# Performance work log

Measured on AMD Instinct MI355X. Metric: run time of the kernel, lower is better.

Reference implementation:

```python
import jax, jax.numpy as jnp
import numpy as np

NUM_HEADS = 8
BN_EPS = 1e-5


def setup_inputs() -> dict:
    key = jax.random.key(0)
    ks = jax.random.split(key, 8)
    B, Ct, Cs, H, W, E = 8, 256, 128, 32, 32, 256
    s = 0.05  # small init scale to keep softmax logits reasonable
    return {
        "tgt": jax.random.normal(ks[0], (B, Ct, H, W), jnp.float32),
        "src": jax.random.normal(ks[1], (B, Cs, H, W), jnp.float32),
        "kv_w": jax.random.normal(ks[2], (E, Cs), jnp.float32) * s,
        "in_proj_w": jax.random.normal(ks[3], (3 * E, E), jnp.float32) * s,
        "in_proj_b": jnp.zeros((3 * E,), jnp.float32),
        "out_proj_w": jax.random.normal(ks[4], (E, E), jnp.float32) * s,
        "out_proj_b": jnp.zeros((E,), jnp.float32),
        "fuse_w": jax.random.normal(ks[5], (Ct, E), jnp.float32) * s,
        "bn_gamma": jnp.ones((Ct,), jnp.float32),
        "bn_beta": jnp.zeros((Ct,), jnp.float32),
        "bn_mean": jnp.zeros((Ct,), jnp.float32),
        "bn_var": jnp.ones((Ct,), jnp.float32),
    }


def reference(tgt, src, kv_w, in_proj_w, in_proj_b, out_proj_w, out_proj_b,
              fuse_w, bn_gamma, bn_beta, bn_mean, bn_var):
    B, Ct, H, W = tgt.shape
    E = kv_w.shape[0]
    nH = NUM_HEADS
    hd = E // nH

    # q_proj is Identity (C_tgt == embed_dim); flatten spatial to tokens [B, Q, E]
    q_seq = tgt.reshape(B, Ct, H * W).transpose(0, 2, 1)
    # kv_proj: 1x1 conv == channel matmul; then flatten to [B, K, E]
    kv_map = jnp.einsum('bchw,ec->behw', src, kv_w)
    k_seq = kv_map.reshape(B, E, H * W).transpose(0, 2, 1)

    # nn.MultiheadAttention: packed in-projection
    Wq, Wk, Wv = in_proj_w[:E], in_proj_w[E:2 * E], in_proj_w[2 * E:]
    bq, bk, bv = in_proj_b[:E], in_proj_b[E:2 * E], in_proj_b[2 * E:]
    qp = (q_seq @ Wq.T + bq).reshape(B, -1, nH, hd).transpose(0, 2, 1, 3)  # [B,h,Q,d]
    kp = (k_seq @ Wk.T + bk).reshape(B, -1, nH, hd).transpose(0, 2, 1, 3)  # [B,h,K,d]
    vp = (k_seq @ Wv.T + bv).reshape(B, -1, nH, hd).transpose(0, 2, 1, 3)  # [B,h,K,d]

    scores = jnp.einsum('bhqd,bhkd->bhqk', qp, kp) / jnp.sqrt(jnp.float32(hd))
    attn = jax.nn.softmax(scores, axis=-1)  # [B,h,Q,K] (non-flash explicit path)

    ctx = jnp.einsum('bhqk,bhkd->bhqd', attn, vp)
    ctx = ctx.transpose(0, 2, 1, 3).reshape(B, -1, E)  # [B,Q,E]
    out_seq = ctx @ out_proj_w.T + out_proj_b

    # cached spatial key-attention map: mean over heads and queries -> [B,1,Hk,Wk]
    attn_map = attn.mean(axis=(1, 2)).reshape(B, 1, H, W)

    # back to map, fuse: 1x1 conv -> BN(eval) -> SiLU, then residual add
    out_map = out_seq.transpose(0, 2, 1).reshape(B, E, H, W)
    fused = jnp.einsum('behw,ce->bchw', out_map, fuse_w)
    inv = bn_gamma / jnp.sqrt(bn_var + BN_EPS)
    bn = (fused - bn_mean[None, :, None, None]) * inv[None, :, None, None] \
         + bn_beta[None, :, None, None]
    y = tgt + bn * jax.nn.sigmoid(bn)  # SiLU
    return y, attn_map
```

## Files before the change

kernel.cpp:

```cpp
#include <hip/hip_runtime.h>
#include <hip/hip_bf16.h>

typedef unsigned short u16;
typedef __attribute__((ext_vector_type(8))) short short8;
typedef __attribute__((ext_vector_type(4))) float f32x4;
typedef __attribute__((ext_vector_type(4))) unsigned short u16x4;

static __device__ __forceinline__ u16 f2bf(float x) {
  __hip_bfloat16 b = __float2bfloat16(x);
  return *reinterpret_cast<u16*>(&b);
}

#define QSCALE 0.17677669529663687f

__global__ __launch_bounds__(256) void prep_kernel(
    const float* __restrict__ in_proj_w, const float* __restrict__ in_proj_b,
    const float* __restrict__ kv_w, const float* __restrict__ fuse_w,
    const float* __restrict__ out_proj_w, const float* __restrict__ out_proj_b,
    const float* __restrict__ gamma, const float* __restrict__ beta,
    const float* __restrict__ mean, const float* __restrict__ var,
    u16* __restrict__ WqB, u16* __restrict__ WkvB, u16* __restrict__ M2B,
    float* __restrict__ qbias, float2* __restrict__ bnpk) {
  int idx = blockIdx.x * 256 + threadIdx.x;
  if (idx < 65536) {
    WqB[idx] = f2bf(in_proj_w[idx] * QSCALE);
  } else if (idx < 131072) {
    int i = idx - 65536;
    int m = i >> 7, c = i & 127;
    const float* wrow = in_proj_w + (size_t)(256 + m) * 256;
    float s = 0.f;
    for (int e2 = 0; e2 < 256; ++e2) s += wrow[e2] * kv_w[e2 * 128 + c];
    WkvB[i] = f2bf(s);
  } else if (idx < 196608) {
    int i = idx - 131072;
    int c = i >> 8, e2 = i & 255;
    float s = 0.f;
    for (int e = 0; e < 256; ++e)
      s += fuse_w[c * 256 + e] * out_proj_w[e * 256 + e2];
    M2B[i] = f2bf(s);
  } else if (idx < 196864) {
    int c = idx - 196608;
    float fbv = 0.f;
    for (int e = 0; e < 256; ++e) fbv += fuse_w[c * 256 + e] * out_proj_b[e];
    float inv = gamma[c] * rsqrtf(var[c] + 1e-5f);
    bnpk[c] = make_float2(inv, (fbv - mean[c]) * inv + beta[c]);
    qbias[c] = in_proj_b[c] * QSCALE;
  }
}

__global__ __launch_bounds__(256, 3) void qkv_gemm(
    const float* __restrict__ tgt, const float* __restrict__ src,
    const u16* __restrict__ WqB, const u16* __restrict__ WkvB,
    const float* __restrict__ qbias, const float* __restrict__ bkv,
    u16* __restrict__ QB, u16* __restrict__ KB, u16* __restrict__ VB) {
  __shared__ __align__(16) u16 Wl[64 * 40];
  __shared__ __align__(16) u16 Xl[128 * 40];
  int b = blockIdx.z, by = blockIdx.y, n0 = blockIdx.x * 128;
  bool isQ = by < 4;
  int m0 = isQ ? by * 64 : (by - 4) * 64;
  int Kd = isQ ? 256 : 128;
  const u16* Wp = isQ ? WqB : WkvB;
  const float* Xp = isQ ? tgt + (size_t)b * 256 * 1024
                        : src + (size_t)b * 128 * 1024;
  int t = threadIdx.x, wave = t >> 6, lane = t & 63;
  int lq = lane & 15, quad = lane >> 4;
  f32x4 acc[4][2];
#pragma unroll
  for (int mt = 0; mt < 4; ++mt)
#pragma unroll
    for (int nt = 0; nt < 2; ++nt) acc[mt][nt] = (f32x4){0.f, 0.f, 0.f, 0.f};

  for (int k0 = 0; k0 < Kd; k0 += 32) {
    __syncthreads();
    {
      int row = t >> 2, seg = t & 3;
      *(short8*)&Wl[row * 40 + seg * 8] =
          *(const short8*)&Wp[(size_t)(m0 + row) * Kd + k0 + seg * 8];
    }
    for (int i = t; i < 4096; i += 256) {
      int k = i >> 7, n = i & 127;
      Xl[n * 40 + k] = f2bf(Xp[(size_t)(k0 + k) * 1024 + n0 + n]);
    }
    __syncthreads();
    short8 af[4], bf[2];
#pragma unroll
    for (int mt = 0; mt < 4; ++mt)
      af[mt] = *(const short8*)&Wl[(mt * 16 + lq) * 40 + quad * 8];
#pragma unroll
    for (int nt = 0; nt < 2; ++nt)
      bf[nt] = *(const short8*)&Xl[(wave * 32 + nt * 16 + lq) * 40 + quad * 8];
#pragma unroll
    for (int mt = 0; mt < 4; ++mt)
#pragma unroll
      for (int nt = 0; nt < 2; ++nt)
        acc[mt][nt] = __builtin_amdgcn_mfma_f32_16x16x32_bf16(af[mt], bf[nt],
                                                              acc[mt][nt], 0, 0, 0);
  }
  if (isQ) {
#pragma unroll
    for (int mt = 0; mt < 4; ++mt) {
      int e = m0 + mt * 16 + quad * 4;
      f32x4 bi = *(const f32x4*)&qbias[e];
#pragma unroll
      for (int nt = 0; nt < 2; ++nt) {
        int n = n0 + wave * 32 + nt * 16 + lq;
        u16x4 pk;
#pragma unroll
        for (int r = 0; r < 4; ++r) pk[r] = f2bf(acc[mt][nt][r] + bi[r]);
        *(u16x4*)&QB[((size_t)b * 1024 + n) * 256 + e] = pk;
      }
    }
  } else {
#pragma unroll
    for (int mt = 0; mt < 4; ++mt) {
      int m = m0 + mt * 16 + quad * 4;
      f32x4 bi = *(const f32x4*)&bkv[m];
#pragma unroll
      for (int nt = 0; nt < 2; ++nt) {
        int n = n0 + wave * 32 + nt * 16 + lq;
        if (m < 256) {
          int hh = m >> 5, d = m & 31;
          u16x4 pk;
#pragma unroll
          for (int r = 0; r < 4; ++r) pk[r] = f2bf(acc[mt][nt][r] + bi[r]);
          *(u16x4*)&KB[((size_t)(b * 8 + hh) * 1024 + n) * 32 + d] = pk;
        } else {
          int e = m - 256;
#pragma unroll
          for (int r = 0; r < 4; ++r)
            VB[((size_t)b * 256 + e + r) * 1024 + n] = f2bf(acc[mt][nt][r] + bi[r]);
        }
      }
    }
  }
}

__global__ __launch_bounds__(256, 4) void attn_mfma(
    const u16* __restrict__ QB, const u16* __restrict__ KB,
    const u16* __restrict__ VB, u16* __restrict__ ctxB,
    float* __restrict__ attn_out) {
  __shared__ __align__(16) u16 Klds[128 * 40];
  __shared__ __align__(16) u16 Vlds[32 * 136];
  __shared__ __align__(16) u16 Plds[4][32 * 40];
  __shared__ float colsum[1024];

  int b = blockIdx.z, h = blockIdx.y, q0 = blockIdx.x * 128;
  int t = threadIdx.x, wave = t >> 6, lane = t & 63;
  int lq = lane & 15, quad = lane >> 4;

  const u16* Qb = QB + (size_t)b * 1024 * 256 + h * 32;
  const u16* Kb = KB + (size_t)(b * 8 + h) * 1024 * 32;
  const u16* Vb = VB + (size_t)(b * 256 + h * 32) * 1024;

  short8 qf[2];
#pragma unroll
  for (int mt = 0; mt < 2; ++mt)
    qf[mt] = *(const short8*)(Qb + (size_t)(q0 + wave * 32 + mt * 16 + lq) * 256 + quad * 8);

  for (int i = t; i < 1024; i += 256) colsum[i] = 0.f;

  float lsum[2][4];
  f32x4 O[2][2];
#pragma unroll
  for (int mt = 0; mt < 2; ++mt) {
#pragma unroll
    for (int r = 0; r < 4; ++r) lsum[mt][r] = 0.f;
#pragma unroll
    for (int nt = 0; nt < 2; ++nt) O[mt][nt] = (f32x4){0.f, 0.f, 0.f, 0.f};
  }
  const f32x4 zf = (f32x4){0.f, 0.f, 0.f, 0.f};
  u16* Pw = &Plds[wave][0];

  for (int c0 = 0; c0 < 1024; c0 += 128) {
    __syncthreads();
    for (int i = t; i < 512; i += 256)
      *(short8*)&Klds[(i >> 2) * 40 + (i & 3) * 8] =
          *(const short8*)(Kb + (size_t)c0 * 32 + i * 8);
    for (int i = t; i < 512; i += 256) {
      int d = i >> 4, part = i & 15;
      *(short8*)&Vlds[d * 136 + part * 8] =
          *(const short8*)(Vb + (size_t)d * 1024 + c0 + part * 8);
    }
    __syncthreads();
#pragma unroll
    for (int pair = 0; pair < 4; ++pair) {
#pragma unroll
      for (int ntp = 0; ntp < 2; ++ntp) {
        int nt = pair * 2 + ntp;
        short8 kf = *(const short8*)&Klds[(nt * 16 + lq) * 40 + quad * 8];
#pragma unroll
        for (int mt = 0; mt < 2; ++mt) {
          f32x4 s = __builtin_amdgcn_mfma_f32_16x16x32_bf16(qf[mt], kf, zf, 0, 0, 0);
#pragma unroll
          for (int r = 0; r < 4; ++r) {
            float e = __expf(s[r]);
            lsum[mt][r] += e;
            Pw[(mt * 16 + quad * 4 + r) * 40 + ntp * 16 + lq] = f2bf(e);
          }
        }
      }
      short8 pf[2], vf[2];
#pragma unroll
      for (int mt = 0; mt < 2; ++mt)
        pf[mt] = *(const short8*)&Pw[(mt * 16 + lq) * 40 + quad * 8];
#pragma unroll
      for (int nt = 0; nt < 2; ++nt)
        vf[nt] = *(const short8*)&Vlds[(nt * 16 + lq) * 136 + pair * 32 + quad * 8];
#pragma unroll
      for (int mt = 0; mt < 2; ++mt)
#pragma unroll
        for (int nt = 0; nt < 2; ++nt)
          O[mt][nt] = __builtin_amdgcn_mfma_f32_16x16x32_bf16(pf[mt], vf[nt],
                                                              O[mt][nt], 0, 0, 0);
    }
  }

  float linv[2][4];
#pragma unroll
  for (int mt = 0; mt < 2; ++mt)
#pragma unroll
    for (int r = 0; r < 4; ++r) {
      float v = lsum[mt][r];
      v += __shfl_xor(v, 1);
      v += __shfl_xor(v, 2);
      v += __shfl_xor(v, 4);
      v += __shfl_xor(v, 8);
      linv[mt][r] = 1.f / v;
    }

#pragma unroll
  for (int mt = 0; mt < 2; ++mt)
#pragma unroll
    for (int nt = 0; nt < 2; ++nt)
#pragma unroll
      for (int r = 0; r < 4; ++r) {
        int q = q0 + wave * 32 + mt * 16 + quad * 4 + r;
        ctxB[((size_t)b * 1024 + q) * 256 + h * 32 + nt * 16 + lq] =
            f2bf(O[mt][nt][r] * linv[mt][r]);
      }

  for (int c0 = 0; c0 < 1024; c0 += 128) {
    __syncthreads();
    for (int i = t; i < 512; i += 256)
      *(short8*)&Klds[(i >> 2) * 40 + (i & 3) * 8] =
          *(const short8*)(Kb + (size_t)c0 * 32 + i * 8);
    __syncthreads();
#pragma unroll
    for (int nt = 0; nt < 8; ++nt) {
      short8 kf = *(const short8*)&Klds[(nt * 16 + lq) * 40 + quad * 8];
      float cs = 0.f;
#pragma unroll
      for (int mt = 0; mt < 2; ++mt) {
        f32x4 s = __builtin_amdgcn_mfma_f32_16x16x32_bf16(qf[mt], kf, zf, 0, 0, 0);
#pragma unroll
        for (int r = 0; r < 4; ++r) cs += __expf(s[r]) * linv[mt][r];
      }
      cs += __shfl_xor(cs, 16);
      cs += __shfl_xor(cs, 32);
      if (quad == 0) atomicAdd(&colsum[c0 + nt * 16 + lq], cs);
    }
  }
  __syncthreads();
  for (int i = t; i < 1024; i += 256)
    atomicAdd(&attn_out[b * 1024 + i], colsum[i] * (1.f / 8192.f));
}

__global__ __launch_bounds__(256, 3) void fused_out(
    const u16* __restrict__ M2B, const u16* __restrict__ ctxB,
    const float* __restrict__ tgt, const float2* __restrict__ bnpk,
    float* __restrict__ y) {
  __shared__ __align__(16) u16 Al[64 * 40];
  __shared__ __align__(16) u16 Bl[128 * 40];
  int b = blockIdx.z, c0 = blockIdx.y * 64, s0 = blockIdx.x * 128;
  int t = threadIdx.x, wave = t >> 6, lane = t & 63;
  int lq = lane & 15, quad = lane >> 4;
  f32x4 acc[4][2];
#pragma unroll
  for (int mt = 0; mt < 4; ++mt)
#pragma unroll
    for (int nt = 0; nt < 2; ++nt) acc[mt][nt] = (f32x4){0.f, 0.f, 0.f, 0.f};

  for (int k0 = 0; k0 < 256; k0 += 32) {
    __syncthreads();
    {
      int row = t >> 2, seg = t & 3;
      *(short8*)&Al[row * 40 + seg * 8] =
          *(const short8*)&M2B[(size_t)(c0 + row) * 256 + k0 + seg * 8];
    }
    for (int i = t; i < 512; i += 256) {
      int row = i >> 2, seg = i & 3;
      *(short8*)&Bl[row * 40 + seg * 8] =
          *(const short8*)&ctxB[((size_t)b * 1024 + s0 + row) * 256 + k0 + seg * 8];
    }
    __syncthreads();
    short8 af[4], bf[2];
#pragma unroll
    for (int mt = 0; mt < 4; ++mt)
      af[mt] = *(const short8*)&Al[(mt * 16 + lq) * 40 + quad * 8];
#pragma unroll
    for (int nt = 0; nt < 2; ++nt)
      bf[nt] = *(const short8*)&Bl[(wave * 32 + nt * 16 + lq) * 40 + quad * 8];
#pragma unroll
    for (int mt = 0; mt < 4; ++mt)
#pragma unroll
      for (int nt = 0; nt < 2; ++nt)
        acc[mt][nt] = __builtin_amdgcn_mfma_f32_16x16x32_bf16(af[mt], bf[nt],
                                                              acc[mt][nt], 0, 0, 0);
  }
#pragma unroll
  for (int mt = 0; mt < 4; ++mt) {
#pragma unroll
    for (int r = 0; r < 4; ++r) {
      int c = c0 + mt * 16 + quad * 4 + r;
      float2 p = bnpk[c];
#pragma unroll
      for (int nt = 0; nt < 2; ++nt) {
        int s = s0 + wave * 32 + nt * 16 + lq;
        float bn = acc[mt][nt][r] * p.x + p.y;
        float sig = 1.f / (1.f + __expf(-bn));
        size_t idx = ((size_t)b * 256 + c) * 1024 + s;
        y[idx] = tgt[idx] + bn * sig;
      }
    }
  }
}

extern "C" void kernel_launch(void* const* d_in, const int* in_sizes, int n_in,
                              void* d_out, int out_size, void* d_ws, size_t ws_size,
                              hipStream_t stream) {
  const float* tgt = (const float*)d_in[0];
  const float* src = (const float*)d_in[1];
  const float* kv_w = (const float*)d_in[2];
  const float* in_proj_w = (const float*)d_in[3];
  const float* in_proj_b = (const float*)d_in[4];
  const float* out_proj_w = (const float*)d_in[5];
  const float* out_proj_b = (const float*)d_in[6];
  const float* fuse_w = (const float*)d_in[7];
  const float* bn_gamma = (const float*)d_in[8];
  const float* bn_beta = (const float*)d_in[9];
  const float* bn_mean = (const float*)d_in[10];
  const float* bn_var = (const float*)d_in[11];

  char* W = (char*)d_ws;
  u16* WqB = (u16*)W;
  u16* WkvB = (u16*)(W + 131072);
  u16* M2B = (u16*)(W + 262144);
  float* qbias = (float*)(W + 393216);
  float2* bnpk = (float2*)(W + 394240);
  u16* QB = (u16*)(W + 397312);
  u16* KB = QB + 2097152;
  u16* VB = KB + 2097152;
  u16* ctxB = VB + 2097152;

  float* y = (float*)d_out;
  float* attn_out = y + 2097152;

  hipMemsetAsync(attn_out, 0, 8192 * sizeof(float), stream);
  prep_kernel<<<769, 256, 0, stream>>>(in_proj_w, in_proj_b, kv_w, fuse_w,
                                       out_proj_w, out_proj_b, bn_gamma, bn_beta,
                                       bn_mean, bn_var, WqB, WkvB, M2B, qbias, bnpk);
  qkv_gemm<<<dim3(8, 12, 8), 256, 0, stream>>>(tgt, src, WqB, WkvB, qbias,
                                               in_proj_b + 256, QB, KB, VB);
  attn_mfma<<<dim3(8, 8, 8), 256, 0, stream>>>(QB, KB, VB, ctxB, attn_out);
  fused_out<<<dim3(8, 4, 8), 256, 0, stream>>>(M2B, ctxB, tgt, bnpk, y);
}
```

Measured before the change: 176.9 us.

## Rewrite attention as register-resident S^T MFMA loop without LDS staging

The attention kernel now computes transposed score tiles (K as the A operand, Q as B), so the exp'd probabilities land in registers already laid out as the B operand of the PV MFMA. That removes the LDS round trip for P and the LDS staging of K and V, which now load straight from global memory. The log2(e) factor is folded into the Q scale so exp2f can replace __expf, and bf16 packing truncates with a byte-permute instead of rounding. Each block now covers 64 queries (16 per wave) over twice as many blocks, trading lower register pressure and no barriers in the main loop for repeated global K/V reads and slightly less accurate bf16 P values.

```diff
diff --git a/kernel.cpp b/kernel.cpp
--- a/kernel.cpp
+++ b/kernel.cpp
@@ -2,16 +2,24 @@
 #include <hip/hip_bf16.h>
 
 typedef unsigned short u16;
+typedef unsigned int u32;
 typedef __attribute__((ext_vector_type(8))) short short8;
 typedef __attribute__((ext_vector_type(4))) float f32x4;
 typedef __attribute__((ext_vector_type(4))) unsigned short u16x4;
+typedef __attribute__((ext_vector_type(4))) int i32x4;
 
 static __device__ __forceinline__ u16 f2bf(float x) {
   __hip_bfloat16 b = __float2bfloat16(x);
   return *reinterpret_cast<u16*>(&b);
 }
-
-#define QSCALE 0.17677669529663687f
+static __device__ __forceinline__ u32 fbits(float x) {
+  union { float f; u32 u; } v; v.f = x; return v.u;
+}
+static __device__ __forceinline__ u32 pk_trunc(float lo, float hi) {
+  return __builtin_amdgcn_perm(fbits(hi), fbits(lo), 0x07060302u);
+}
+
+#define QSCALE2 (0.17677669529663687f * 1.4426950408889634f)
 
 __global__ __launch_bounds__(256) void prep_kernel(
     const float* __restrict__ in_proj_w, const float* __restrict__ in_proj_b,
@@ -23,7 +31,7 @@
     float* __restrict__ qbias, float2* __restrict__ bnpk) {
   int idx = blockIdx.x * 256 + threadIdx.x;
   if (idx < 65536) {
-    WqB[idx] = f2bf(in_proj_w[idx] * QSCALE);
+    WqB[idx] = f2bf(in_proj_w[idx] * QSCALE2);
   } else if (idx < 131072) {
     int i = idx - 65536;
     int m = i >> 7, c = i & 127;
@@ -44,7 +52,7 @@
     for (int e = 0; e < 256; ++e) fbv += fuse_w[c * 256 + e] * out_proj_b[e];
     float inv = gamma[c] * rsqrtf(var[c] + 1e-5f);
     bnpk[c] = make_float2(inv, (fbv - mean[c]) * inv + beta[c]);
-    qbias[c] = in_proj_b[c] * QSCALE;
+    qbias[c] = in_proj_b[c] * QSCALE2;
   }
 }
 
@@ -135,16 +143,12 @@
   }
 }
 
-__global__ __launch_bounds__(256, 4) void attn_mfma(
+__global__ __launch_bounds__(256) void attn_st(
     const u16* __restrict__ QB, const u16* __restrict__ KB,
     const u16* __restrict__ VB, u16* __restrict__ ctxB,
     float* __restrict__ attn_out) {
-  __shared__ __align__(16) u16 Klds[128 * 40];
-  __shared__ __align__(16) u16 Vlds[32 * 136];
-  __shared__ __align__(16) u16 Plds[4][32 * 40];
   __shared__ float colsum[1024];
-
-  int b = blockIdx.z, h = blockIdx.y, q0 = blockIdx.x * 128;
+  int b = blockIdx.z, h = blockIdx.y, q0 = blockIdx.x * 64;
   int t = threadIdx.x, wave = t >> 6, lane = t & 63;
   int lq = lane & 15, quad = lane >> 4;
 
@@ -152,113 +156,77 @@
   const u16* Kb = KB + (size_t)(b * 8 + h) * 1024 * 32;
   const u16* Vb = VB + (size_t)(b * 256 + h * 32) * 1024;
 
-  short8 qf[2];
-#pragma unroll
-  for (int mt = 0; mt < 2; ++mt)
-    qf[mt] = *(const short8*)(Qb + (size_t)(q0 + wave * 32 + mt * 16 + lq) * 256 + quad * 8);
-
   for (int i = t; i < 1024; i += 256) colsum[i] = 0.f;
 
-  float lsum[2][4];
-  f32x4 O[2][2];
-#pragma unroll
-  for (int mt = 0; mt < 2; ++mt) {
-#pragma unroll
-    for (int r = 0; r < 4; ++r) lsum[mt][r] = 0.f;
-#pragma unroll
-    for (int nt = 0; nt < 2; ++nt) O[mt][nt] = (f32x4){0.f, 0.f, 0.f, 0.f};
-  }
+  int myq = q0 + wave * 16 + lq;
+  short8 qf = *(const short8*)(Qb + (size_t)myq * 256 + quad * 8);
+
+  int keyA = ((lq >> 2) << 3) | (lq & 3);
+  const u16* KbA0 = Kb + (size_t)keyA * 32 + quad * 8;
+  const u16* KbA1 = Kb + (size_t)(keyA + 4) * 32 + quad * 8;
+  const u16* Vb0 = Vb + (size_t)lq * 1024 + quad * 8;
+  const u16* Vb1 = Vb + (size_t)(16 + lq) * 1024 + quad * 8;
+
   const f32x4 zf = (f32x4){0.f, 0.f, 0.f, 0.f};
-  u16* Pw = &Plds[wave][0];
-
-  for (int c0 = 0; c0 < 1024; c0 += 128) {
-    __syncthreads();
-    for (int i = t; i < 512; i += 256)
-      *(short8*)&Klds[(i >> 2) * 40 + (i & 3) * 8] =
-          *(const short8*)(Kb + (size_t)c0 * 32 + i * 8);
-    for (int i = t; i < 512; i += 256) {
-      int d = i >> 4, part = i & 15;
-      *(short8*)&Vlds[d * 136 + part * 8] =
-          *(const short8*)(Vb + (size_t)d * 1024 + c0 + part * 8);
-    }
-    __syncthreads();
-#pragma unroll
-    for (int pair = 0; pair < 4; ++pair) {
-#pragma unroll
-      for (int ntp = 0; ntp < 2; ++ntp) {
-        int nt = pair * 2 + ntp;
-        short8 kf = *(const short8*)&Klds[(nt * 16 + lq) * 40 + quad * 8];
-#pragma unroll
-        for (int mt = 0; mt < 2; ++mt) {
-          f32x4 s = __builtin_amdgcn_mfma_f32_16x16x32_bf16(qf[mt], kf, zf, 0, 0, 0);
-#pragma unroll
-          for (int r = 0; r < 4; ++r) {
-            float e = __expf(s[r]);
-            lsum[mt][r] += e;
-            Pw[(mt * 16 + quad * 4 + r) * 40 + ntp * 16 + lq] = f2bf(e);
-          }
-        }
-      }
-      short8 pf[2], vf[2];
-#pragma unroll
-      for (int mt = 0; mt < 2; ++mt)
-        pf[mt] = *(const short8*)&Pw[(mt * 16 + lq) * 40 + quad * 8];
-#pragma unroll
-      for (int nt = 0; nt < 2; ++nt)
-        vf[nt] = *(const short8*)&Vlds[(nt * 16 + lq) * 136 + pair * 32 + quad * 8];
-#pragma unroll
-      for (int mt = 0; mt < 2; ++mt)
-#pragma unroll
-        for (int nt = 0; nt < 2; ++nt)
-          O[mt][nt] = __builtin_amdgcn_mfma_f32_16x16x32_bf16(pf[mt], vf[nt],
-                                                              O[mt][nt], 0, 0, 0);
-    }
-  }
-
-  float linv[2][4];
-#pragma unroll
-  for (int mt = 0; mt < 2; ++mt)
+  f32x4 O0 = zf, O1 = zf;
+  float lsum = 0.f;
+
+#pragma unroll 2
+  for (int c = 0; c < 1024; c += 32) {
+    short8 kf0 = *(const short8*)(KbA0 + (size_t)c * 32);
+    short8 kf1 = *(const short8*)(KbA1 + (size_t)c * 32);
+    f32x4 s0 = __builtin_amdgcn_mfma_f32_16x16x32_bf16(kf0, qf, zf, 0, 0, 0);
+    f32x4 s1 = __builtin_amdgcn_mfma_f32_16x16x32_bf16(kf1, qf, zf, 0, 0, 0);
+    f32x4 e0, e1;
 #pragma unroll
     for (int r = 0; r < 4; ++r) {
-      float v = lsum[mt][r];
-      v += __shfl_xor(v, 1);
-      v += __shfl_xor(v, 2);
-      v += __shfl_xor(v, 4);
-      v += __shfl_xor(v, 8);
-      linv[mt][r] = 1.f / v;
-    }
-
-#pragma unroll
-  for (int mt = 0; mt < 2; ++mt)
-#pragma unroll
-    for (int nt = 0; nt < 2; ++nt)
-#pragma unroll
-      for (int r = 0; r < 4; ++r) {
-        int q = q0 + wave * 32 + mt * 16 + quad * 4 + r;
-        ctxB[((size_t)b * 1024 + q) * 256 + h * 32 + nt * 16 + lq] =
-            f2bf(O[mt][nt][r] * linv[mt][r]);
-      }
-
-  for (int c0 = 0; c0 < 1024; c0 += 128) {
-    __syncthreads();
-    for (int i = t; i < 512; i += 256)
-      *(short8*)&Klds[(i >> 2) * 40 + (i & 3) * 8] =
-          *(const short8*)(Kb + (size_t)c0 * 32 + i * 8);
-    __syncthreads();
-#pragma unroll
-    for (int nt = 0; nt < 8; ++nt) {
-      short8 kf = *(const short8*)&Klds[(nt * 16 + lq) * 40 + quad * 8];
-      float cs = 0.f;
-#pragma unroll
-      for (int mt = 0; mt < 2; ++mt) {
-        f32x4 s = __builtin_amdgcn_mfma_f32_16x16x32_bf16(qf[mt], kf, zf, 0, 0, 0);
-#pragma unroll
-        for (int r = 0; r < 4; ++r) cs += __expf(s[r]) * linv[mt][r];
-      }
-      cs += __shfl_xor(cs, 16);
-      cs += __shfl_xor(cs, 32);
-      if (quad == 0) atomicAdd(&colsum[c0 + nt * 16 + lq], cs);
-    }
+      e0[r] = exp2f(s0[r]);
+      e1[r] = exp2f(s1[r]);
+    }
+    lsum += (e0[0] + e0[1]) + (e0[2] + e0[3]) + (e1[0] + e1[1]) + (e1[2] + e1[3]);
+    i32x4 pi;
+    pi[0] = (int)pk_trunc(e0[0], e0[1]);
+    pi[1] = (int)pk_trunc(e0[2], e0[3]);
+    pi[2] = (int)pk_trunc(e1[0], e1[1]);
+    pi[3] = (int)pk_trunc(e1[2], e1[3]);
+    short8 pf = *(short8*)&pi;
+    short8 vf0 = *(const short8*)(Vb0 + c);
+    short8 vf1 = *(const short8*)(Vb1 + c);
+    O0 = __builtin_amdgcn_mfma_f32_16x16x32_bf16(vf0, pf, O0, 0, 0, 0);
+    O1 = __builtin_amdgcn_mfma_f32_16x16x32_bf16(vf1, pf, O1, 0, 0, 0);
+  }
+
+  lsum += __shfl_xor(lsum, 16);
+  lsum += __shfl_xor(lsum, 32);
+  float linv = 1.f / lsum;
+
+  {
+    u16x4 pk0, pk1;
+#pragma unroll
+    for (int r = 0; r < 4; ++r) {
+      pk0[r] = f2bf(O0[r] * linv);
+      pk1[r] = f2bf(O1[r] * linv);
+    }
+    u16* crow = ctxB + ((size_t)b * 1024 + myq) * 256 + h * 32 + quad * 4;
+    *(u16x4*)crow = pk0;
+    *(u16x4*)(crow + 16) = pk1;
+  }
+
+  float lv[4];
+#pragma unroll
+  for (int r = 0; r < 4; ++r) lv[r] = __shfl(linv, quad * 4 + r);
+
+  __syncthreads();
+
+#pragma unroll 2
+  for (int c = 0; c < 1024; c += 16) {
+    short8 kf = *(const short8*)(Kb + (size_t)(c + lq) * 32 + quad * 8);
+    f32x4 s = __builtin_amdgcn_mfma_f32_16x16x32_bf16(qf, kf, zf, 0, 0, 0);
+    float cs = exp2f(s[0]) * lv[0] + exp2f(s[1]) * lv[1] +
+               exp2f(s[2]) * lv[2] + exp2f(s[3]) * lv[3];
+    cs += __shfl_xor(cs, 16);
+    cs += __shfl_xor(cs, 32);
+    if (quad == 0) atomicAdd(&colsum[c + lq], cs);
   }
   __syncthreads();
   for (int i = t; i < 1024; i += 256)
@@ -361,6 +329,6 @@
                                        bn_mean, bn_var, WqB, WkvB, M2B, qbias, bnpk);
   qkv_gemm<<<dim3(8, 12, 8), 256, 0, stream>>>(tgt, src, WqB, WkvB, qbias,
                                                in_proj_b + 256, QB, KB, VB);
-  attn_mfma<<<dim3(8, 8, 8), 256, 0, stream>>>(QB, KB, VB, ctxB, attn_out);
+  attn_st<<<dim3(16, 8, 8), 256, 0, stream>>>(QB, KB, VB, ctxB, attn_out);
   fused_out<<<dim3(8, 4, 8), 256, 0, stream>>>(M2B, ctxB, tgt, bnpk, y);
 }
```

After: 203.8 us. +15.2%, slower.
